# Performance work log

Hardware: AMD Instinct MI355X
Metric: run time of the kernel (lower is better)

Reference implementation:

```python
import jax, jax.numpy as jnp
import numpy as np

EMBEDS = 512
HEADS = 4
HEAD_SIZE = 512  # head_size = embeds in Block.__init__
D_HEAD = EMBEDS // HEADS  # 128
LN_EPS = 512.0  # nn.LayerNorm(embeds, head_size) -> eps=head_size (faithful to source bug)
B, T = 4096, 4  # T must equal heads=4 for the mask broadcast in the source to work


def layer_norm(x, g, b, eps=LN_EPS):
    mu = jnp.mean(x, axis=-1, keepdims=True)
    var = jnp.mean(jnp.square(x - mu), axis=-1, keepdims=True)
    return (x - mu) / jnp.sqrt(var + eps) * g + b


def setup_inputs() -> dict:
    key = jax.random.key(0)
    ks = jax.random.split(key, 12)
    s_qkv = 1.0 / np.sqrt(D_HEAD)
    s_proj = 1.0 / np.sqrt(HEAD_SIZE)
    s_ff1 = 1.0 / np.sqrt(EMBEDS)
    s_ff2 = 1.0 / np.sqrt(4 * EMBEDS)
    return {
        "x": jax.random.normal(ks[0], (B, T, EMBEDS), dtype=jnp.float32),
        "Wq": jax.random.uniform(ks[1], (D_HEAD, HEAD_SIZE), jnp.float32, -s_qkv, s_qkv),
        "Wk": jax.random.uniform(ks[2], (D_HEAD, HEAD_SIZE), jnp.float32, -s_qkv, s_qkv),
        "Wv": jax.random.uniform(ks[3], (D_HEAD, HEAD_SIZE), jnp.float32, -s_qkv, s_qkv),
        "Wp": jax.random.uniform(ks[4], (HEAD_SIZE, EMBEDS), jnp.float32, -s_proj, s_proj),
        "bp": jax.random.uniform(ks[5], (EMBEDS,), jnp.float32, -s_proj, s_proj),
        "W1": jax.random.uniform(ks[6], (EMBEDS, 4 * EMBEDS), jnp.float32, -s_ff1, s_ff1),
        "b1": jax.random.uniform(ks[7], (4 * EMBEDS,), jnp.float32, -s_ff1, s_ff1),
        "W2": jax.random.uniform(ks[8], (4 * EMBEDS, EMBEDS), jnp.float32, -s_ff2, s_ff2),
        "b2": jax.random.uniform(ks[9], (EMBEDS,), jnp.float32, -s_ff2, s_ff2),
        "ln1_g": jnp.ones((EMBEDS,), jnp.float32),
        "ln1_b": jnp.zeros((EMBEDS,), jnp.float32),
        "ln2_g": jnp.ones((EMBEDS,), jnp.float32),
        "ln2_b": jnp.zeros((EMBEDS,), jnp.float32),
    }


def reference(x, Wq, Wk, Wv, Wp, bp, W1, b1, W2, b2, ln1_g, ln1_b, ln2_g, ln2_b):
    Bx, Tx, C = x.shape
    xh = x.reshape(Bx, Tx, HEADS, C // HEADS)          # [B,T,4,128]
    q = jnp.einsum('bthc,cd->bthd', xh, Wq)            # [B,T,4,512]
    k = jnp.einsum('bthc,cd->bthd', xh, Wk)
    v = jnp.einsum('bthc,cd->bthd', xh, Wv)
    # scores over the HEAD axis (faithful to source): [B,T,4,4]
    wei = jnp.einsum('btid,btjd->btij', q, k) * (HEAD_SIZE ** -0.5)
    causal = jnp.tril(jnp.ones((Tx, Tx), dtype=bool))  # broadcast over trailing [4,4]; requires T==4
    wei = jnp.where(causal, wei, -jnp.inf)
    wei = jax.nn.softmax(wei, axis=-1)                 # dropout omitted (eval mode)
    att = jnp.einsum('btij,btjd->btid', wei, v)        # [B,T,4,512]
    y = jnp.einsum('btid,de->btie', att, Wp) + bp      # [B,T,4,512]
    # residual broadcast: x [B,T,512] + y [B,T,4,512] -> [B,T,4,512]
    x1 = layer_norm(x[:, :, None, :] + y, ln1_g, ln1_b)
    h = jax.nn.gelu(jnp.einsum('btie,ef->btif', x1, W1) + b1, approximate=False)
    h = jnp.einsum('btif,fe->btie', h, W2) + b2
    return layer_norm(x1 + h, ln2_g, ln2_b)            # [B,T,4,512]
```

## Files before the change

### kernel.cpp

```cpp
#include <hip/hip_runtime.h>
#include <hip/hip_bf16.h>
#include <math.h>

typedef __bf16 bf16x8 __attribute__((ext_vector_type(8)));
typedef float f32x4 __attribute__((ext_vector_type(4)));
typedef unsigned short u16;
typedef unsigned int u32;
typedef u16 u16x4 __attribute__((ext_vector_type(4)));
typedef u16 u16x8 __attribute__((ext_vector_type(8)));

#define TOKENS 16384
#define MROWS  65536

__device__ __forceinline__ u16 f2bf(float f) {
  union { __hip_bfloat16 h; u16 u; } c;
  c.h = __float2bfloat16(f);
  return c.u;
}
__device__ __forceinline__ float bf2f(u16 u) {
  union { u16 u; __hip_bfloat16 h; } c;
  c.u = u;
  return __bfloat162float(c.h);
}
__device__ __forceinline__ float gelu_f(float u) {
  float y2 = u * fmaf(0.07135481283f, u * u, 1.595769122f);
  float e = __expf(-y2);
  return u / (1.f + e);
}
__device__ __forceinline__ void gload16(const void* g, void* l) {
  __builtin_amdgcn_global_load_lds(
      (const __attribute__((address_space(1))) void*)g,
      (__attribute__((address_space(3))) void*)l, 16, 0, 0);
}

__global__ void kprep_G(const float* __restrict__ Wq, const float* __restrict__ Wk,
                        u16* __restrict__ Gbf) {
  int id = blockIdx.x * 256 + threadIdx.x;
  int c = id >> 7, c2 = id & 127;
  const float4* a = (const float4*)(Wq + (size_t)c * 512);
  const float4* b = (const float4*)(Wk + (size_t)c2 * 512);
  float s = 0.f;
#pragma unroll 8
  for (int i = 0; i < 128; ++i) {
    float4 xa = a[i], yb = b[i];
    s += xa.x * yb.x + xa.y * yb.y + xa.z * yb.z + xa.w * yb.w;
  }
  Gbf[id] = f2bf(s * 0.044194173824159216f);
}

__global__ void kprep_Wvp(const float* __restrict__ Wv, const float* __restrict__ Wp,
                          u16* __restrict__ WvpT) {
  int id = blockIdx.x * 256 + threadIdx.x;
  int e = id >> 7, c = id & 127;
  float s = 0.f;
#pragma unroll 4
  for (int d = 0; d < 512; ++d) s += Wv[(size_t)c * 512 + d] * Wp[(size_t)d * 512 + e];
  WvpT[id] = f2bf(s);
}

__global__ __launch_bounds__(256) void kprep_W1T(const float* __restrict__ W1,
                                                 u16* __restrict__ W1T) {
  __shared__ u16 Lt[64][72];
  int tid = threadIdx.x;
  int bf = blockIdx.x, be = blockIdx.y;
#pragma unroll
  for (int rnd = 0; rnd < 4; ++rnd) {
    int r = rnd * 16 + (tid >> 4);
    int f4 = (tid & 15) * 4;
    float4 v = *(const float4*)(W1 + (size_t)(be * 64 + r) * 2048 + bf * 64 + f4);
    Lt[r][f4] = f2bf(v.x); Lt[r][f4 + 1] = f2bf(v.y);
    Lt[r][f4 + 2] = f2bf(v.z); Lt[r][f4 + 3] = f2bf(v.w);
  }
  __syncthreads();
  int fl = tid >> 2, eg = (tid & 3) * 16;
  u16x8 o0, o1;
#pragma unroll
  for (int q = 0; q < 8; ++q) { o0[q] = Lt[eg + q][fl]; o1[q] = Lt[eg + 8 + q][fl]; }
  u16* dst = W1T + (size_t)(bf * 64 + fl) * 512 + be * 64 + eg;
  *(u16x8*)dst = o0;
  *(u16x8*)(dst + 8) = o1;
}

__global__ __launch_bounds__(256) void kprep_W2T(const float* __restrict__ W2,
                                                 u16* __restrict__ W2T) {
  __shared__ u16 Lt[64][72];
  int tid = threadIdx.x;
  int bf = blockIdx.x, be = blockIdx.y;
#pragma unroll
  for (int rnd = 0; rnd < 4; ++rnd) {
    int r = rnd * 16 + (tid >> 4);
    int e4 = (tid & 15) * 4;
    float4 v = *(const float4*)(W2 + (size_t)(bf * 64 + r) * 512 + be * 64 + e4);
    Lt[r][e4] = f2bf(v.x); Lt[r][e4 + 1] = f2bf(v.y);
    Lt[r][e4 + 2] = f2bf(v.z); Lt[r][e4 + 3] = f2bf(v.w);
  }
  __syncthreads();
  int aa = bf & 1, fb = bf >> 1;
  int el = tid >> 2, g = tid & 3;
  u16x8 o0, o1;
#pragma unroll
  for (int q = 0; q < 8; ++q) {
    int fs0 = g * 16 + q, fs1 = g * 16 + 8 + q;
    o0[q] = Lt[(fs0 & 3) * 16 + ((fs0 >> 2) & 15)][el];
    o1[q] = Lt[(fs1 & 3) * 16 + ((fs1 >> 2) & 15)][el];
  }
  u16* dst = W2T + (size_t)(be * 64 + el) * 2048 + fb * 128 + aa * 64 + g * 16;
  *(u16x8*)dst = o0;
  *(u16x8*)(dst + 8) = o1;
}

__global__ __launch_bounds__(256) void ktoken(const float* __restrict__ x,
                                              const u16* __restrict__ Gbf,
                                              u16* __restrict__ Z) {
  __shared__ float Ss[4 * 512];
  __shared__ __align__(16) u16 Gs[16384];
  int tid = threadIdx.x;
  int wave = tid >> 6, lane = tid & 63;
  int tok = blockIdx.x * 4 + wave;
  char* GsC = (char*)Gs;
#pragma unroll
  for (int it = 0; it < 8; ++it)
    gload16(Gbf + (size_t)(it * 256 + tid) * 8, GsC + it * 4096 + wave * 1024);
  {
    const float4* xs = (const float4*)(x + (size_t)tok * 512);
    float4* sw = (float4*)(Ss + wave * 512);
    sw[lane] = xs[lane];
    sw[64 + lane] = xs[64 + lane];
  }
  __syncthreads();

  const float* Sw = Ss + wave * 512;
  const u32* Grow = (const u32*)Gs;
  float a[4][2] = {{0.f, 0.f}, {0.f, 0.f}, {0.f, 0.f}, {0.f, 0.f}};
#pragma unroll 4
  for (int c = 0; c < 128; ++c) {
    u32 g2 = Grow[c * 64 + lane];
    float glo = __uint_as_float(g2 << 16);
    float ghi = __uint_as_float(g2 & 0xFFFF0000u);
    float s0 = Sw[c], s1 = Sw[128 + c], s2 = Sw[256 + c], s3 = Sw[384 + c];
    a[0][0] += s0 * glo; a[0][1] += s0 * ghi;
    a[1][0] += s1 * glo; a[1][1] += s1 * ghi;
    a[2][0] += s2 * glo; a[2][1] += s2 * ghi;
    a[3][0] += s3 * glo; a[3][1] += s3 * ghi;
  }
  float w[16];
#pragma unroll
  for (int j = 0; j < 4; ++j) {
    float sj0 = Sw[j * 128 + 2 * lane];
    float sj1 = Sw[j * 128 + 2 * lane + 1];
#pragma unroll
    for (int i = 0; i < 4; ++i)
      w[i * 4 + j] = a[i][0] * sj0 + a[i][1] * sj1;
  }
#pragma unroll
  for (int off = 1; off < 64; off <<= 1)
#pragma unroll
    for (int k = 0; k < 16; ++k) w[k] += __shfl_xor(w[k], off);
  float p[4][4];
#pragma unroll
  for (int i = 0; i < 4; ++i) {
    float m = w[i * 4];
    for (int j = 1; j <= i; ++j) m = fmaxf(m, w[i * 4 + j]);
    float s = 0.f;
    for (int j = 0; j <= i; ++j) { p[i][j] = __expf(w[i * 4 + j] - m); s += p[i][j]; }
    float inv = 1.f / s;
    for (int j = 0; j <= i; ++j) p[i][j] *= inv;
    for (int j = i + 1; j < 4; ++j) p[i][j] = 0.f;
  }
  int c = lane * 2;
  u32* zout = (u32*)(Z + (size_t)tok * 512);
#pragma unroll
  for (int i = 0; i < 4; ++i) {
    float z0 = 0.f, z1 = 0.f;
#pragma unroll
    for (int j = 0; j < 4; ++j) {
      z0 += p[i][j] * Sw[j * 128 + c];
      z1 += p[i][j] * Sw[j * 128 + c + 1];
    }
    zout[i * 64 + lane] = (u32)f2bf(z0) | ((u32)f2bf(z1) << 16);
  }
}

__global__ __launch_bounds__(512) void kattn(const u16* __restrict__ Z,
                                             const u16* __restrict__ WvpT,
                                             const float* __restrict__ bp,
                                             const float* __restrict__ x,
                                             const float* __restrict__ g1,
                                             const float* __restrict__ bln1,
                                             u16* __restrict__ X1) {
  __shared__ u16 AO[32768];
  __shared__ float rsum[64 * 4];
  __shared__ float rsq[64 * 4];
  __shared__ float mus[64];
  __shared__ float rss[64];
  char* smem = (char*)AO;
  int tid = threadIdx.x;
  int lane = tid & 63, wid = tid >> 6;
  int wm = wid >> 2, wnq = wid & 3;
  int lane_lo = lane & 15, lane_hi = lane >> 4;
  int m0 = blockIdx.x * 64;
  {
    const bf16x8* src = (const bf16x8*)(Z + (size_t)m0 * 128);
#pragma unroll
    for (int it = 0; it < 2; ++it) {
      int idx8 = it * 512 + tid;
      int row = idx8 >> 4;
      int byte = (idx8 * 16) ^ ((row & 7) << 4);
      *(bf16x8*)(smem + byte) = src[idx8];
    }
  }
  __syncthreads();
  f32x4 acc[2][8];
#pragma unroll
  for (int mi = 0; mi < 2; ++mi)
#pragma unroll
    for (int ni = 0; ni < 8; ++ni) acc[mi][ni] = (f32x4){0.f, 0.f, 0.f, 0.f};
#pragma unroll
  for (int ks = 0; ks < 4; ++ks) {
    bf16x8 af[2];
#pragma unroll
    for (int mi = 0; mi < 2; ++mi) {
      int row = wm * 32 + mi * 16 + lane_lo;
      int byte = (row * 256 + (ks * 32 + lane_hi * 8) * 2) ^ ((row & 7) << 4);
      af[mi] = *(const bf16x8*)(smem + byte);
    }
#pragma unroll
    for (int ni = 0; ni < 8; ++ni) {
      int n = wnq * 128 + ni * 16 + lane_lo;
      bf16x8 bfr = *(const bf16x8*)(WvpT + (size_t)n * 128 + ks * 32 + lane_hi * 8);
#pragma unroll
      for (int mi = 0; mi < 2; ++mi)
        acc[mi][ni] = __builtin_amdgcn_mfma_f32_16x16x32_bf16(af[mi], bfr, acc[mi][ni], 0, 0, 0);
    }
  }
#pragma unroll
  for (int mi = 0; mi < 2; ++mi) {
#pragma unroll
    for (int j = 0; j < 4; ++j) {
      int rl = wm * 32 + mi * 16 + lane_hi * 4 + j;
      int R = m0 + rl;
      const float* xrow = x + (size_t)(R >> 2) * 512;
      float s = 0.f, q = 0.f;
#pragma unroll
      for (int ni = 0; ni < 8; ++ni) {
        int col = wnq * 128 + ni * 16 + lane_lo;
        float val = acc[mi][ni][j] + bp[col] + xrow[col];
        acc[mi][ni][j] = val;
        s += val; q += val * val;
      }
#pragma unroll
      for (int off = 1; off < 16; off <<= 1) { s += __shfl_xor(s, off); q += __shfl_xor(q, off); }
      if (lane_lo == 0) { rsum[rl * 4 + wnq] = s; rsq[rl * 4 + wnq] = q; }
    }
  }
  __syncthreads();
  if (tid < 64) {
    float s = rsum[tid * 4] + rsum[tid * 4 + 1] + rsum[tid * 4 + 2] + rsum[tid * 4 + 3];
    float q = rsq[tid * 4] + rsq[tid * 4 + 1] + rsq[tid * 4 + 2] + rsq[tid * 4 + 3];
    float mu = s * (1.f / 512.f);
    float var = q * (1.f / 512.f) - mu * mu;
    mus[tid] = mu;
    rss[tid] = rsqrtf(var + 512.0f);
  }
  __syncthreads();
#pragma unroll
  for (int mi = 0; mi < 2; ++mi) {
#pragma unroll
    for (int j = 0; j < 4; ++j) {
      int rl = wm * 32 + mi * 16 + lane_hi * 4 + j;
      float mu = mus[rl], rs = rss[rl];
#pragma unroll
      for (int ni = 0; ni < 8; ++ni) {
        int col = wnq * 128 + ni * 16 + lane_lo;
        AO[rl * 512 + col] = f2bf((acc[mi][ni][j] - mu) * rs * g1[col] + bln1[col]);
      }
    }
  }
  __syncthreads();
  {
    bf16x8* dst = (bf16x8*)(X1 + (size_t)m0 * 512);
    const bf16x8* s8 = (const bf16x8*)AO;
#pragma unroll
    for (int it = 0; it < 8; ++it) dst[it * 512 + tid] = s8[it * 512 + tid];
  }
}

template<int KDIM>
__device__ __forceinline__ void gemm_core_sb(const u16* __restrict__ Ap,
                                             const u16* __restrict__ Bp,
                                             u16* Ab, u16* Bb,
                                             int wid, int lane, f32x4 acc[4][4]) {
  const int lane_lo = lane & 15, lane_hi = lane >> 4;
  const int wm = wid >> 1, wn = wid & 1;
  const int rl8 = lane >> 3, u8 = lane & 7;
  char* AbC = (char*)Ab;
  char* BbC = (char*)Bb;
  for (int k0 = 0; k0 < KDIM; k0 += 64) {
#pragma unroll
    for (int i = 0; i < 4; ++i) {
      int row = wid * 32 + i * 8 + rl8;
      int usw = u8 ^ (row & 7);
      size_t goff = (size_t)row * KDIM + k0 + usw * 8;
      gload16(Ap + goff, AbC + wid * 4096 + i * 1024);
      gload16(Bp + goff, BbC + wid * 4096 + i * 1024);
    }
    __syncthreads();
#pragma unroll
    for (int ks = 0; ks < 2; ++ks) {
      bf16x8 av[4], bv[4];
#pragma unroll
      for (int mi = 0; mi < 4; ++mi) {
        int row = wm * 64 + mi * 16 + lane_lo;
        int usw = (ks * 4 + lane_hi) ^ (row & 7);
        av[mi] = *(const bf16x8*)(AbC + row * 128 + usw * 16);
      }
#pragma unroll
      for (int ni = 0; ni < 4; ++ni) {
        int row = wn * 64 + ni * 16 + lane_lo;
        int usw = (ks * 4 + lane_hi) ^ (row & 7);
        bv[ni] = *(const bf16x8*)(BbC + row * 128 + usw * 16);
      }
#pragma unroll
      for (int mi = 0; mi < 4; ++mi)
#pragma unroll
        for (int ni = 0; ni < 4; ++ni)
          acc[mi][ni] = __builtin_amdgcn_mfma_f32_16x16x32_bf16(av[mi], bv[ni], acc[mi][ni], 0, 0, 0);
    }
    __syncthreads();
  }
}

template<int KDIM>
__device__ __forceinline__ void gemm_core_db(const u16* __restrict__ Ap,
                                             const u16* __restrict__ Bp,
                                             u16* AbBase, u16* BbBase,
                                             int wid, int lane, f32x4 acc[4][4]) {
  const int lane_lo = lane & 15, lane_hi = lane >> 4;
  const int wm = wid >> 1, wn = wid & 1;
  const int rl8 = lane >> 3, u8 = lane & 7;

  auto stage = [&](int buf, int k0) {
    char* AbC = (char*)AbBase + buf * 16384;
    char* BbC = (char*)BbBase + buf * 16384;
#pragma unroll
    for (int i = 0; i < 4; ++i) {
      int row = wid * 32 + i * 8 + rl8;
      int usw = u8 ^ (row & 7);
      size_t goff = (size_t)row * KDIM + k0 + usw * 8;
      gload16(Ap + goff, AbC + wid * 4096 + i * 1024);
      gload16(Bp + goff, BbC + wid * 4096 + i * 1024);
    }
  };
  auto compute = [&](int buf) {
    char* AbC = (char*)AbBase + buf * 16384;
    char* BbC = (char*)BbBase + buf * 16384;
#pragma unroll
    for (int ks = 0; ks < 2; ++ks) {
      bf16x8 av[4], bv[4];
#pragma unroll
      for (int mi = 0; mi < 4; ++mi) {
        int row = wm * 64 + mi * 16 + lane_lo;
        int usw = (ks * 4 + lane_hi) ^ (row & 7);
        av[mi] = *(const bf16x8*)(AbC + row * 128 + usw * 16);
      }
#pragma unroll
      for (int ni = 0; ni < 4; ++ni) {
        int row = wn * 64 + ni * 16 + lane_lo;
        int usw = (ks * 4 + lane_hi) ^ (row & 7);
        bv[ni] = *(const bf16x8*)(BbC + row * 128 + usw * 16);
      }
#pragma unroll
      for (int mi = 0; mi < 4; ++mi)
#pragma unroll
        for (int ni = 0; ni < 4; ++ni)
          acc[mi][ni] = __builtin_amdgcn_mfma_f32_16x16x32_bf16(av[mi], bv[ni], acc[mi][ni], 0, 0, 0);
    }
  };

  stage(0, 0);
  asm volatile("s_waitcnt vmcnt(0)" ::: "memory");
  __builtin_amdgcn_s_barrier();
  __builtin_amdgcn_sched_barrier(0);
  int cur = 0;
  for (int k0 = 64; k0 < KDIM; k0 += 64) {
    stage(cur ^ 1, k0);
    compute(cur);
    asm volatile("s_waitcnt vmcnt(0)" ::: "memory");
    __builtin_amdgcn_s_barrier();
    __builtin_amdgcn_sched_barrier(0);
    cur ^= 1;
  }
  compute(cur);
}

__global__ __launch_bounds__(256) void kff1(const u16* __restrict__ X1s,
                                            const u16* __restrict__ W1T,
                                            const float* __restrict__ b1v,
                                            u16* __restrict__ H) {
  __shared__ __align__(16) u16 Ab[8192];
  __shared__ __align__(16) u16 Bb[8192];
  int tid = threadIdx.x, lane = tid & 63, wid = tid >> 6;
  int nwg = gridDim.x, bid = blockIdx.x;
  int m128 = nwg >> 4;
  int xcd = bid & 7, idx = bid >> 3;
  int mb = xcd * (m128 >> 3) + (idx >> 4);
  int nb = idx & 15;
  const u16* Ap = X1s + (size_t)mb * 128 * 512;
  const u16* Bp = W1T + (size_t)nb * 128 * 512;
  f32x4 acc[4][4];
#pragma unroll
  for (int mi = 0; mi < 4; ++mi)
#pragma unroll
    for (int ni = 0; ni < 4; ++ni) acc[mi][ni] = (f32x4){0.f, 0.f, 0.f, 0.f};
  gemm_core_sb<512>(Ap, Bp, Ab, Bb, wid, lane, acc);
  int lane_lo = lane & 15, lane_hi = lane >> 4;
  int wm = wid >> 1, wn = wid & 1;
  float bvals[4];
#pragma unroll
  for (int ni = 0; ni < 4; ++ni) bvals[ni] = b1v[nb * 128 + wn * 64 + ni * 16 + lane_lo];
  int colb = nb * 128 + (wn * 16 + lane_lo) * 4;
#pragma unroll
  for (int mi = 0; mi < 4; ++mi)
#pragma unroll
    for (int j = 0; j < 4; ++j) {
      int rl = wm * 64 + mi * 16 + lane_hi * 4 + j;
      u16x4 pk;
#pragma unroll
      for (int ni = 0; ni < 4; ++ni)
        pk[ni] = f2bf(gelu_f(acc[mi][ni][j] + bvals[ni]));
      *(u16x4*)(H + ((size_t)mb * 128 + rl) * 2048 + colb) = pk;
    }
}

__global__ __launch_bounds__(256) void kff2(const u16* __restrict__ H,
                                            const u16* __restrict__ W2T,
                                            const float* __restrict__ b2v,
                                            const u16* __restrict__ X1s,
                                            float* __restrict__ Ps) {
  __shared__ __align__(16) u16 Ab[16384];
  __shared__ __align__(16) u16 Bb[16384];
  int tid = threadIdx.x, lane = tid & 63, wid = tid >> 6;
  int nwg = gridDim.x, bid = blockIdx.x;
  int m128 = nwg >> 2;
  int xcd = bid & 7, idx = bid >> 3;
  int mb = xcd * (m128 >> 3) + (idx >> 2);
  int nb = idx & 3;
  const u16* Ap = H + (size_t)mb * 128 * 2048;
  const u16* Bp = W2T + (size_t)nb * 128 * 2048;
  f32x4 acc[4][4];
#pragma unroll
  for (int mi = 0; mi < 4; ++mi)
#pragma unroll
    for (int ni = 0; ni < 4; ++ni) acc[mi][ni] = (f32x4){0.f, 0.f, 0.f, 0.f};
  gemm_core_db<2048>(Ap, Bp, Ab, Bb, wid, lane, acc);
  int lane_lo = lane & 15, lane_hi = lane >> 4;
  int wm = wid >> 1, wn = wid & 1;
#pragma unroll
  for (int mi = 0; mi < 4; ++mi)
#pragma unroll
    for (int j = 0; j < 4; ++j) {
      int rl = wm * 64 + mi * 16 + lane_hi * 4 + j;
      size_t row = (size_t)mb * 128 + rl;
      const u16* xrow = X1s + row * 512 + nb * 128;
      float* prow = Ps + row * 512 + nb * 128;
#pragma unroll
      for (int ni = 0; ni < 4; ++ni) {
        int col = wn * 64 + ni * 16 + lane_lo;
        prow[col] = acc[mi][ni][j] + b2v[nb * 128 + col] + bf2f(xrow[col]);
      }
    }
}

__global__ __launch_bounds__(512) void kln2(float* __restrict__ P,
                                            const float* __restrict__ g2,
                                            const float* __restrict__ bb2) {
  int wid = threadIdx.x >> 6, lane = threadIdx.x & 63;
  size_t row = (size_t)blockIdx.x * 8 + wid;
  float* pr = P + row * 512;
  float4 v0 = *(float4*)(pr + lane * 4);
  float4 v1 = *(float4*)(pr + 256 + lane * 4);
  float s = v0.x + v0.y + v0.z + v0.w + v1.x + v1.y + v1.z + v1.w;
  float q = v0.x * v0.x + v0.y * v0.y + v0.z * v0.z + v0.w * v0.w +
            v1.x * v1.x + v1.y * v1.y + v1.z * v1.z + v1.w * v1.w;
#pragma unroll
  for (int off = 1; off < 64; off <<= 1) { s += __shfl_xor(s, off); q += __shfl_xor(q, off); }
  float mu = s * (1.f / 512.f);
  float rs = rsqrtf(q * (1.f / 512.f) - mu * mu + 512.0f);
  float4 ga = *(const float4*)(g2 + lane * 4);
  float4 gb = *(const float4*)(g2 + 256 + lane * 4);
  float4 ba = *(const float4*)(bb2 + lane * 4);
  float4 bb = *(const float4*)(bb2 + 256 + lane * 4);
  v0.x = (v0.x - mu) * rs * ga.x + ba.x;
  v0.y = (v0.y - mu) * rs * ga.y + ba.y;
  v0.z = (v0.z - mu) * rs * ga.z + ba.z;
  v0.w = (v0.w - mu) * rs * ga.w + ba.w;
  v1.x = (v1.x - mu) * rs * gb.x + bb.x;
  v1.y = (v1.y - mu) * rs * gb.y + bb.y;
  v1.z = (v1.z - mu) * rs * gb.z + bb.z;
  v1.w = (v1.w - mu) * rs * gb.w + bb.w;
  *(float4*)(pr + lane * 4) = v0;
  *(float4*)(pr + 256 + lane * 4) = v1;
}

extern "C" void kernel_launch(void* const* d_in, const int* in_sizes, int n_in,
                              void* d_out, int out_size, void* d_ws, size_t ws_size,
                              hipStream_t stream) {
  const float* x   = (const float*)d_in[0];
  const float* Wq  = (const float*)d_in[1];
  const float* Wk  = (const float*)d_in[2];
  const float* Wv  = (const float*)d_in[3];
  const float* Wp  = (const float*)d_in[4];
  const float* bp  = (const float*)d_in[5];
  const float* W1  = (const float*)d_in[6];
  const float* b1  = (const float*)d_in[7];
  const float* W2  = (const float*)d_in[8];
  const float* b2  = (const float*)d_in[9];
  const float* g1  = (const float*)d_in[10];
  const float* bb1 = (const float*)d_in[11];
  const float* g2  = (const float*)d_in[12];
  const float* bb2 = (const float*)d_in[13];
  float* out = (float*)d_out;

  char* ws = (char*)d_ws;
  u16* Gbf  = (u16*)ws;
  u16* WvpT = (u16*)(ws + (256 << 10));
  u16* W1T  = (u16*)(ws + (1 << 20));
  u16* W2T  = (u16*)(ws + (3 << 20));
  u16* Z    = (u16*)(ws + (5 << 20));
  u16* X1   = (u16*)(ws + (21 << 20));
  u16* H    = (u16*)(ws + (85ull << 20));

  hipLaunchKernelGGL(kprep_G,   dim3(64),        dim3(256), 0, stream, Wq, Wk, Gbf);
  hipLaunchKernelGGL(kprep_Wvp, dim3(256),       dim3(256), 0, stream, Wv, Wp, WvpT);
  hipLaunchKernelGGL(kprep_W1T, dim3(32, 8),     dim3(256), 0, stream, W1, W1T);
  hipLaunchKernelGGL(kprep_W2T, dim3(32, 8),     dim3(256), 0, stream, W2, W2T);
  hipLaunchKernelGGL(ktoken,    dim3(4096),      dim3(256), 0, stream, x, Gbf, Z);
  hipLaunchKernelGGL(kattn,     dim3(1024),      dim3(512), 0, stream, Z, WvpT, bp, x, g1, bb1, X1);

  const size_t hbase = 85ull << 20;
  int S = 64;
  for (int c = 4; c <= 64; c <<= 1) {
    if (hbase + (268435456ull / (size_t)c) <= ws_size) { S = c; break; }
  }
  int Ms = MROWS / S;
  for (int s = 0; s < S; ++s) {
    const u16* x1s = X1 + (size_t)s * Ms * 512;
    float* outs = out + (size_t)s * Ms * 512;
    hipLaunchKernelGGL(kff1, dim3((Ms / 128) * 16), dim3(256), 0, stream, x1s, W1T, b1, H);
    hipLaunchKernelGGL(kff2, dim3((Ms / 128) * 4),  dim3(256), 0, stream, H, W2T, b2, x1s, outs);
  }
  hipLaunchKernelGGL(kln2, dim3(8192), dim3(512), 0, stream, out, g2, bb2);
}
```

Baseline: 631.8 us.

## Stage x rows in LDS for attention epilogue and keep FF2 residual in bf16

The attention kernel now brings Z and the matching x rows into shared memory with gload16 before the GEMM, and holds bias and LN gain/shift in registers. Before, x, bp, g1 and bln1 were reloaded from global memory for every element. The FF2 epilogue now writes its bf16 residual sum in place into X1 rather than an fp32 scratch copy of the output, and kln2 reads that bf16 buffer and writes fp32 once. This roughly halves intermediate traffic but rounds the pre-LN2 sum to bf16, which costs some accuracy.

```diff
diff --git a/kernel.cpp b/kernel.cpp
--- a/kernel.cpp
+++ b/kernel.cpp
@@ -188,7 +188,7 @@
                                              const float* __restrict__ g1,
                                              const float* __restrict__ bln1,
                                              u16* __restrict__ X1) {
-  __shared__ u16 AO[32768];
+  __shared__ __align__(16) u16 AO[32768];
   __shared__ float rsum[64 * 4];
   __shared__ float rsq[64 * 4];
   __shared__ float mus[64];
@@ -200,13 +200,18 @@
   int lane_lo = lane & 15, lane_hi = lane >> 4;
   int m0 = blockIdx.x * 64;
   {
-    const bf16x8* src = (const bf16x8*)(Z + (size_t)m0 * 128);
+    const u16* Zs = Z + (size_t)m0 * 128;
 #pragma unroll
     for (int it = 0; it < 2; ++it) {
       int idx8 = it * 512 + tid;
-      int row = idx8 >> 4;
-      int byte = (idx8 * 16) ^ ((row & 7) << 4);
-      *(bf16x8*)(smem + byte) = src[idx8];
+      int row = idx8 >> 4, u = idx8 & 15;
+      gload16(Zs + (size_t)row * 128 + ((u ^ (row & 7)) << 3), smem + idx8 * 16);
+    }
+    const float* xsrc = x + (size_t)(m0 >> 2) * 512;
+#pragma unroll
+    for (int it = 0; it < 4; ++it) {
+      int idx = it * 512 + tid;
+      gload16(xsrc + idx * 4, smem + 16384 + idx * 16);
     }
   }
   __syncthreads();
@@ -233,18 +238,24 @@
         acc[mi][ni] = __builtin_amdgcn_mfma_f32_16x16x32_bf16(af[mi], bfr, acc[mi][ni], 0, 0, 0);
     }
   }
+  float bpv[8], g1v[8], blv[8];
+#pragma unroll
+  for (int ni = 0; ni < 8; ++ni) {
+    int col = wnq * 128 + ni * 16 + lane_lo;
+    bpv[ni] = bp[col]; g1v[ni] = g1[col]; blv[ni] = bln1[col];
+  }
+  const float* xs = (const float*)(smem + 16384);
 #pragma unroll
   for (int mi = 0; mi < 2; ++mi) {
 #pragma unroll
     for (int j = 0; j < 4; ++j) {
       int rl = wm * 32 + mi * 16 + lane_hi * 4 + j;
-      int R = m0 + rl;
-      const float* xrow = x + (size_t)(R >> 2) * 512;
+      int tl = wm * 8 + mi * 4 + lane_hi;
       float s = 0.f, q = 0.f;
 #pragma unroll
       for (int ni = 0; ni < 8; ++ni) {
         int col = wnq * 128 + ni * 16 + lane_lo;
-        float val = acc[mi][ni][j] + bp[col] + xrow[col];
+        float val = acc[mi][ni][j] + bpv[ni] + xs[tl * 512 + col];
         acc[mi][ni][j] = val;
         s += val; q += val * val;
       }
@@ -272,7 +283,7 @@
 #pragma unroll
       for (int ni = 0; ni < 8; ++ni) {
         int col = wnq * 128 + ni * 16 + lane_lo;
-        AO[rl * 512 + col] = f2bf((acc[mi][ni][j] - mu) * rs * g1[col] + bln1[col]);
+        AO[rl * 512 + col] = f2bf((acc[mi][ni][j] - mu) * rs * g1v[ni] + blv[ni]);
       }
     }
   }
@@ -435,8 +446,7 @@
 __global__ __launch_bounds__(256) void kff2(const u16* __restrict__ H,
                                             const u16* __restrict__ W2T,
                                             const float* __restrict__ b2v,
-                                            const u16* __restrict__ X1s,
-                                            float* __restrict__ Ps) {
+                                            u16* __restrict__ X1y) {
   __shared__ __align__(16) u16 Ab[16384];
   __shared__ __align__(16) u16 Bb[16384];
   int tid = threadIdx.x, lane = tid & 63, wid = tid >> 6;
@@ -461,45 +471,50 @@
     for (int j = 0; j < 4; ++j) {
       int rl = wm * 64 + mi * 16 + lane_hi * 4 + j;
       size_t row = (size_t)mb * 128 + rl;
-      const u16* xrow = X1s + row * 512 + nb * 128;
-      float* prow = Ps + row * 512 + nb * 128;
+      u16* xrow = X1y + row * 512 + nb * 128;
 #pragma unroll
       for (int ni = 0; ni < 4; ++ni) {
         int col = wn * 64 + ni * 16 + lane_lo;
-        prow[col] = acc[mi][ni][j] + b2v[nb * 128 + col] + bf2f(xrow[col]);
-      }
-    }
-}
-
-__global__ __launch_bounds__(512) void kln2(float* __restrict__ P,
+        float val = acc[mi][ni][j] + b2v[nb * 128 + col] + bf2f(xrow[col]);
+        xrow[col] = f2bf(val);
+      }
+    }
+}
+
+__global__ __launch_bounds__(512) void kln2(const u16* __restrict__ Y,
                                             const float* __restrict__ g2,
-                                            const float* __restrict__ bb2) {
+                                            const float* __restrict__ bb2,
+                                            float* __restrict__ out) {
   int wid = threadIdx.x >> 6, lane = threadIdx.x & 63;
   size_t row = (size_t)blockIdx.x * 8 + wid;
-  float* pr = P + row * 512;
-  float4 v0 = *(float4*)(pr + lane * 4);
-  float4 v1 = *(float4*)(pr + 256 + lane * 4);
-  float s = v0.x + v0.y + v0.z + v0.w + v1.x + v1.y + v1.z + v1.w;
-  float q = v0.x * v0.x + v0.y * v0.y + v0.z * v0.z + v0.w * v0.w +
-            v1.x * v1.x + v1.y * v1.y + v1.z * v1.z + v1.w * v1.w;
+  u16x8 v = *(const u16x8*)(Y + row * 512 + lane * 8);
+  float f[8];
+  float s = 0.f, q = 0.f;
+#pragma unroll
+  for (int k = 0; k < 8; ++k) {
+    f[k] = bf2f(v[k]);
+    s += f[k]; q += f[k] * f[k];
+  }
 #pragma unroll
   for (int off = 1; off < 64; off <<= 1) { s += __shfl_xor(s, off); q += __shfl_xor(q, off); }
   float mu = s * (1.f / 512.f);
   float rs = rsqrtf(q * (1.f / 512.f) - mu * mu + 512.0f);
-  float4 ga = *(const float4*)(g2 + lane * 4);
-  float4 gb = *(const float4*)(g2 + 256 + lane * 4);
-  float4 ba = *(const float4*)(bb2 + lane * 4);
-  float4 bb = *(const float4*)(bb2 + 256 + lane * 4);
-  v0.x = (v0.x - mu) * rs * ga.x + ba.x;
-  v0.y = (v0.y - mu) * rs * ga.y + ba.y;
-  v0.z = (v0.z - mu) * rs * ga.z + ba.z;
-  v0.w = (v0.w - mu) * rs * ga.w + ba.w;
-  v1.x = (v1.x - mu) * rs * gb.x + bb.x;
-  v1.y = (v1.y - mu) * rs * gb.y + bb.y;
-  v1.z = (v1.z - mu) * rs * gb.z + bb.z;
-  v1.w = (v1.w - mu) * rs * gb.w + bb.w;
-  *(float4*)(pr + lane * 4) = v0;
-  *(float4*)(pr + 256 + lane * 4) = v1;
+  float4 ga = *(const float4*)(g2 + lane * 8);
+  float4 gb = *(const float4*)(g2 + lane * 8 + 4);
+  float4 ba = *(const float4*)(bb2 + lane * 8);
+  float4 bb = *(const float4*)(bb2 + lane * 8 + 4);
+  float4 o0, o1;
+  o0.x = (f[0] - mu) * rs * ga.x + ba.x;
+  o0.y = (f[1] - mu) * rs * ga.y + ba.y;
+  o0.z = (f[2] - mu) * rs * ga.z + ba.z;
+  o0.w = (f[3] - mu) * rs * ga.w + ba.w;
+  o1.x = (f[4] - mu) * rs * gb.x + bb.x;
+  o1.y = (f[5] - mu) * rs * gb.y + bb.y;
+  o1.z = (f[6] - mu) * rs * gb.z + bb.z;
+  o1.w = (f[7] - mu) * rs * gb.w + bb.w;
+  float* orow = out + row * 512 + lane * 8;
+  *(float4*)orow = o0;
+  *(float4*)(orow + 4) = o1;
 }
 
 extern "C" void kernel_launch(void* const* d_in, const int* in_sizes, int n_in,
@@ -545,9 +560,9 @@
   int Ms = MROWS / S;
   for (int s = 0; s < S; ++s) {
     const u16* x1s = X1 + (size_t)s * Ms * 512;
-    float* outs = out + (size_t)s * Ms * 512;
     hipLaunchKernelGGL(kff1, dim3((Ms / 128) * 16), dim3(256), 0, stream, x1s, W1T, b1, H);
-    hipLaunchKernelGGL(kff2, dim3((Ms / 128) * 4),  dim3(256), 0, stream, H, W2T, b2, x1s, outs);
-  }
-  hipLaunchKernelGGL(kln2, dim3(8192), dim3(512), 0, stream, out, g2, bb2);
-}
+    hipLaunchKernelGGL(kff2, dim3((Ms / 128) * 4),  dim3(256), 0, stream, H, W2T, b2,
+                       X1 + (size_t)s * Ms * 512);
+  }
+  hipLaunchKernelGGL(kln2, dim3(8192), dim3(512), 0, stream, X1, g2, bb2, out);
+}
```

Result: faster. 596.6 us (-5.6%).
